# Kernel tuning notes

Hardware: AMD Instinct MI355X
Metric: run time of the kernel (lower is better)

Reference implementation:

```python
import jax, jax.numpy as jnp
import numpy as np

D_MODEL = 2048
D_HID = D_MODEL // 2
NUM_EXPERTS = 16
TOP_K = 2
EPS = 1e-8


def setup_inputs() -> dict:
    key = jax.random.key(0)
    k1, k2, k3, k4, k5 = jax.random.split(key, 5)
    hidden_states = jax.random.normal(k1, (8, 4096, D_MODEL), dtype=jnp.float32)
    # Linear layers: PyTorch stores weight as [out, in]; we keep [in, out] for x @ W.
    s1 = 1.0 / np.sqrt(D_MODEL)
    s2 = 1.0 / np.sqrt(D_HID)
    W1 = jax.random.uniform(k2, (D_MODEL, D_HID), jnp.float32, -s1, s1)
    b1 = jax.random.uniform(k3, (D_HID,), jnp.float32, -s1, s1)
    W2 = jax.random.uniform(k4, (D_HID, NUM_EXPERTS), jnp.float32, -s2, s2)
    b2 = jax.random.uniform(k5, (NUM_EXPERTS,), jnp.float32, -s2, s2)
    return {"hidden_states": hidden_states, "W1": W1, "b1": b1, "W2": W2, "b2": b2}


def reference(hidden_states, W1, b1, W2, b2):
    # 2-layer MLP router (dropout in eval mode -> identity)
    h = jax.nn.relu(jnp.einsum("bsd,dh->bsh", hidden_states, W1) + b1)
    logits = jnp.einsum("bsh,he->bse", h, W2) + b2  # [B, S, E]
    router_probs = jax.nn.softmax(logits, axis=-1)
    top_k_gates, top_k_indices = jax.lax.top_k(router_probs, TOP_K)
    top_k_gates = top_k_gates / (jnp.sum(top_k_gates, axis=-1, keepdims=True) + EPS)
    return top_k_gates, top_k_indices, router_probs
```

## Files before the change

kernel.cpp:

```cpp
#include <hip/hip_runtime.h>
#include <math.h>
#include <stdint.h>

#define TOKENS 32768
#define DM 2048
#define DH 1024
#define NE 16
#define BM 128
#define BN 512
#define NPASS 2
#define BK 32
#define NSTAGE 64
#define RT_TAU 5e-5f
#define FB_TAU 5e-4f
#define XSC 16.0f
#define WSC 64.0f
#define DESC (1.0f/1024.0f)

#define OFF_IDX  (TOKENS * 2)
#define OFF_PROB (TOKENS * 4)

#define WS_LIST 1024
#define WS_WT   132096
#define WIMG_BYTES ((size_t)NSTAGE * NPASS * 65536)
#define WS_NEEDED ((size_t)WS_WT + WIMG_BYTES)
#define RCAP 512

typedef _Float16 f16x8 __attribute__((ext_vector_type(8)));
typedef short    bf16x8 __attribute__((ext_vector_type(8)));
typedef float    f32x16 __attribute__((ext_vector_type(16)));

static __device__ __forceinline__ void gload_lds16(const void* g, void* l) {
    __builtin_amdgcn_global_load_lds(
        (const __attribute__((address_space(1))) void*)g,
        (__attribute__((address_space(3))) void*)l, 16, 0, 0);
}

static __device__ __forceinline__ void cvt_split8(float4 u, float4 v, f16x8& hi, f16x8& lo) {
    float f[8] = {u.x * XSC, u.y * XSC, u.z * XSC, u.w * XSC,
                  v.x * XSC, v.y * XSC, v.z * XSC, v.w * XSC};
    #pragma unroll
    for (int j = 0; j < 8; ++j) {
        _Float16 h = (_Float16)f[j];
        hi[j] = h;
        lo[j] = (_Float16)(f[j] - (float)h);
    }
}

__global__ __launch_bounds__(256)
void prep_w16(const float* __restrict__ W1, char* __restrict__ wimg) {
    const int bid = blockIdx.x;
    const int s = bid >> 1, p = bid & 1;
    char* img = wimg + ((size_t)bid << 16);
    const int tid = threadIdx.x;
    #pragma unroll
    for (int rep = 0; rep < 2; ++rep) {
        const int n = tid + rep * 256;
        #pragma unroll
        for (int q = 0; q < 4; ++q) {
            f16x8 hi, lo;
            #pragma unroll
            for (int j = 0; j < 8; ++j) {
                float ww = W1[(size_t)(s * 32 + q * 8 + j) * DH + p * 512 + n] * WSC;
                _Float16 h = (_Float16)ww;
                hi[j] = h;
                lo[j] = (_Float16)(ww - (float)h);
            }
            *(f16x8*)(img + ((q * 2 + 0) * 512 + n) * 16) = hi;
            *(f16x8*)(img + ((q * 2 + 1) * 512 + n) * 16) = lo;
        }
    }
}

__global__ __launch_bounds__(512, 2)
void router16(const float* __restrict__ x, const char* __restrict__ wimg,
              const float* __restrict__ b1, const float* __restrict__ W2,
              const float* __restrict__ b2, float* __restrict__ out,
              int* __restrict__ cnt, int* __restrict__ list)
{
    __shared__ __align__(16) char smem[163840];
    float* h_lds = (float*)smem;
    float* w2t   = (float*)(smem + 65536);
    float* ls    = (float*)(smem + 73728);
    float* lsred = (float*)smem;

    const int tid  = threadIdx.x;
    const int wid  = tid >> 6;
    const int lane = tid & 63;
    const int l31  = lane & 31;
    const int lh   = lane >> 5;
    const int wm   = wid >> 2;
    const int wn   = wid & 3;
    const int m0   = blockIdx.x * BM;

    const int tq  = tid & 31;
    const int egq = (tid >> 5) & 3;
    const int ns  = tid >> 7;

    const int arow = tid >> 2, kq = tid & 3;

    float lacc[4][4];
    #pragma unroll
    for (int i = 0; i < 4; ++i)
        #pragma unroll
        for (int e = 0; e < 4; ++e) lacc[i][e] = 0.f;

    for (int p = 0; p < NPASS; ++p) {
        f32x16 acc[2][4];
        #pragma unroll
        for (int mf = 0; mf < 2; ++mf)
            #pragma unroll
            for (int nf = 0; nf < 4; ++nf)
                #pragma unroll
                for (int q = 0; q < 16; ++q) acc[mf][nf][q] = 0.f;

        {
            const char* img = wimg + ((size_t)(0 * 2 + p) << 16);
            #pragma unroll
            for (int i = 0; i < 8; ++i) {
                int seg = (wid << 3) + i;
                gload_lds16(img + (seg << 10) + (lane << 4), smem + (seg << 10));
            }
            const float* xp = x + (size_t)(m0 + arow) * DM + kq * 8;
            float4 u = *(const float4*)xp;
            float4 v = *(const float4*)(xp + 4);
            f16x8 hi, lo;
            cvt_split8(u, v, hi, lo);
            char* ab = smem + 131072;
            *(f16x8*)(ab + ((kq * 2 + 0) * 128 + arow) * 16) = hi;
            *(f16x8*)(ab + ((kq * 2 + 1) * 128 + arow) * 16) = lo;
        }
        __syncthreads();

        for (int s = 0; s < NSTAGE; ++s) {
            const int cur = s & 1;
            float4 xu, xv;
            if (s < NSTAGE - 1) {
                const char* img = wimg + ((size_t)((s + 1) * 2 + p) << 16);
                #pragma unroll
                for (int i = 0; i < 8; ++i) {
                    int seg = (wid << 3) + i;
                    gload_lds16(img + (seg << 10) + (lane << 4),
                                smem + ((cur ^ 1) << 16) + (seg << 10));
                }
                const float* xp = x + (size_t)(m0 + arow) * DM + (s + 1) * BK + kq * 8;
                xu = *(const float4*)xp;
                xv = *(const float4*)(xp + 4);
            }
            const char* bb = smem + (cur << 16);
            const char* ab = smem + 131072 + (cur << 14);
            {
                const int q = lh;
                f16x8 ah[2], al[2], bh[4], bl[4];
                #pragma unroll
                for (int mf = 0; mf < 2; ++mf) {
                    int m = wm * 64 + mf * 32 + l31;
                    ah[mf] = *(const f16x8*)(ab + ((q * 2 + 0) * 128 + m) * 16);
                    al[mf] = *(const f16x8*)(ab + ((q * 2 + 1) * 128 + m) * 16);
                }
                #pragma unroll
                for (int nf = 0; nf < 4; ++nf) {
                    int n = wn * 128 + nf * 32 + l31;
                    bh[nf] = *(const f16x8*)(bb + ((q * 2 + 0) * 512 + n) * 16);
                    bl[nf] = *(const f16x8*)(bb + ((q * 2 + 1) * 512 + n) * 16);
                }
                #pragma unroll
                for (int mf = 0; mf < 2; ++mf)
                    #pragma unroll
                    for (int nf = 0; nf < 4; ++nf) {
                        acc[mf][nf] = __builtin_amdgcn_mfma_f32_32x32x16_f16(ah[mf], bh[nf], acc[mf][nf], 0, 0, 0);
                        acc[mf][nf] = __builtin_amdgcn_mfma_f32_32x32x16_f16(ah[mf], bl[nf], acc[mf][nf], 0, 0, 0);
                        acc[mf][nf] = __builtin_amdgcn_mfma_f32_32x32x16_f16(al[mf], bh[nf], acc[mf][nf], 0, 0, 0);
                    }
            }
            if (s < NSTAGE - 1) {
                f16x8 hi, lo;
                cvt_split8(xu, xv, hi, lo);
                char* abn = smem + 131072 + ((cur ^ 1) << 14);
                *(f16x8*)(abn + ((kq * 2 + 0) * 128 + arow) * 16) = hi;
                *(f16x8*)(abn + ((kq * 2 + 1) * 128 + arow) * 16) = lo;
            }
            {
                const int q = 2 + lh;
                f16x8 ah[2], al[2], bh[4], bl[4];
                #pragma unroll
                for (int mf = 0; mf < 2; ++mf) {
                    int m = wm * 64 + mf * 32 + l31;
                    ah[mf] = *(const f16x8*)(ab + ((q * 2 + 0) * 128 + m) * 16);
                    al[mf] = *(const f16x8*)(ab + ((q * 2 + 1) * 128 + m) * 16);
                }
                #pragma unroll
                for (int nf = 0; nf < 4; ++nf) {
                    int n = wn * 128 + nf * 32 + l31;
                    bh[nf] = *(const f16x8*)(bb + ((q * 2 + 0) * 512 + n) * 16);
                    bl[nf] = *(const f16x8*)(bb + ((q * 2 + 1) * 512 + n) * 16);
                }
                #pragma unroll
                for (int mf = 0; mf < 2; ++mf)
                    #pragma unroll
                    for (int nf = 0; nf < 4; ++nf) {
                        acc[mf][nf] = __builtin_amdgcn_mfma_f32_32x32x16_f16(ah[mf], bh[nf], acc[mf][nf], 0, 0, 0);
                        acc[mf][nf] = __builtin_amdgcn_mfma_f32_32x32x16_f16(ah[mf], bl[nf], acc[mf][nf], 0, 0, 0);
                        acc[mf][nf] = __builtin_amdgcn_mfma_f32_32x32x16_f16(al[mf], bh[nf], acc[mf][nf], 0, 0, 0);
                    }
            }
            __syncthreads();
        }
        __syncthreads();

        for (int ch = 0; ch < 4; ++ch) {
            __syncthreads();
            if (wn == ch) {
                #pragma unroll
                for (int nf = 0; nf < 4; ++nf) {
                    int col = nf * 32 + l31;
                    float bb2 = b1[p * BN + ch * 128 + col];
                    #pragma unroll
                    for (int mf = 0; mf < 2; ++mf)
                        #pragma unroll
                        for (int r = 0; r < 16; ++r) {
                            int row = wm * 64 + mf * 32 + (r & 3) + 8 * (r >> 2) + 4 * lh;
                            h_lds[row * 128 + col] = fmaxf(acc[mf][nf][r] * DESC + bb2, 0.f);
                        }
                }
            }
            #pragma unroll
            for (int q = 0; q < 4; ++q) {
                int i = tid * 4 + q;
                int nn = i >> 4, e = i & 15;
                w2t[e * 128 + nn] = W2[(size_t)(p * BN + ch * 128 + nn) * NE + e];
            }
            __syncthreads();
            for (int nn = 0; nn < 32; ++nn) {
                int nL = ns * 32 + ((nn + tq) & 31);
                float hv[4], wv[4];
                #pragma unroll
                for (int i = 0; i < 4; ++i) hv[i] = h_lds[(tq * 4 + i) * 128 + nL];
                #pragma unroll
                for (int e = 0; e < 4; ++e) wv[e] = w2t[(egq * 4 + e) * 128 + nL];
                #pragma unroll
                for (int i = 0; i < 4; ++i)
                    #pragma unroll
                    for (int e = 0; e < 4; ++e)
                        lacc[i][e] = fmaf(hv[i], wv[e], lacc[i][e]);
            }
        }
        __syncthreads();
    }

    #pragma unroll
    for (int i = 0; i < 4; ++i)
        #pragma unroll
        for (int e = 0; e < 4; ++e)
            lsred[((tq * 4 + i) * 16 + egq * 4 + e) * 4 + ns] = lacc[i][e];
    __syncthreads();
    #pragma unroll
    for (int q = 0; q < 4; ++q) {
        int idx = tid * 4 + q;
        int t = idx >> 4, e = idx & 15;
        ls[t * 17 + e] = lsred[idx * 4 + 0] + lsred[idx * 4 + 1] +
                         lsred[idx * 4 + 2] + lsred[idx * 4 + 3] + b2[e];
    }
    __syncthreads();

    if (tid < BM) {
        int t = tid;
        float l[NE]; float mx = -1e30f;
        #pragma unroll
        for (int e = 0; e < NE; ++e) { l[e] = ls[t * 17 + e]; mx = fmaxf(mx, l[e]); }
        float pb[NE]; float ssum = 0.f;
        #pragma unroll
        for (int e = 0; e < NE; ++e) { pb[e] = expf(l[e] - mx); ssum += pb[e]; }
        float inv = 1.f / ssum;
        #pragma unroll
        for (int e = 0; e < NE; ++e) pb[e] *= inv;

        int i1 = 0; float p1 = pb[0];
        #pragma unroll
        for (int e = 1; e < NE; ++e) if (pb[e] > p1) { p1 = pb[e]; i1 = e; }
        int i2 = -1; float p2 = -1.f;
        #pragma unroll
        for (int e = 0; e < NE; ++e) if (e != i1 && pb[e] > p2) { p2 = pb[e]; i2 = e; }
        float p3 = -1.f;
        #pragma unroll
        for (int e = 0; e < NE; ++e) if (e != i1 && e != i2 && pb[e] > p3) p3 = pb[e];

        float denom = p1 + p2 + 1e-8f;
        size_t gt = (size_t)(m0 + t);
        out[gt * 2 + 0] = p1 / denom;
        out[gt * 2 + 1] = p2 / denom;
        out[OFF_IDX + gt * 2 + 0] = (float)i1;
        out[OFF_IDX + gt * 2 + 1] = (float)i2;
        #pragma unroll
        for (int e = 0; e < NE; ++e) out[OFF_PROB + gt * 16 + e] = pb[e];

        if (p1 - p2 < RT_TAU || p2 - p3 < RT_TAU) {
            int k = atomicAdd(cnt, 1);
            list[k] = m0 + t;
        }
    }
}

__global__ __launch_bounds__(256, 4)
void repair_partial(const float* __restrict__ x, const float* __restrict__ W1,
                    const int* __restrict__ cnt, const int* __restrict__ list,
                    float* __restrict__ hpart)
{
    __shared__ float xsl[4][512];
    __shared__ int tokid[4];
    const int tid = threadIdx.x;
    int nrep = cnt[0]; if (nrep > RCAP) nrep = RCAP;
    const int g = blockIdx.x >> 2, ks = blockIdx.x & 3;
    if (g * 4 >= nrep) return;

    if (tid < 4) {
        int j = g * 4 + tid;
        tokid[tid] = list[j < nrep ? j : 0];
    }
    __syncthreads();
    #pragma unroll
    for (int i = 0; i < 2; ++i) {
        int slot = tid + i * 256;
        int t = slot >> 7, c = slot & 127;
        *(float4*)(&xsl[t][c * 4]) =
            *(const float4*)(x + (size_t)tokid[t] * DM + ks * 512 + c * 4);
    }
    __syncthreads();

    float acc[4][4];
    #pragma unroll
    for (int t = 0; t < 4; ++t)
        #pragma unroll
        for (int q = 0; q < 4; ++q) acc[t][q] = 0.f;

    for (int k4 = 0; k4 < 128; ++k4) {
        float4 xv[4];
        #pragma unroll
        for (int t = 0; t < 4; ++t) xv[t] = *(const float4*)(&xsl[t][k4 * 4]);
        #pragma unroll
        for (int kk = 0; kk < 4; ++kk) {
            const float4 w = *(const float4*)(W1 + (size_t)(ks * 512 + k4 * 4 + kk) * DH + tid * 4);
            #pragma unroll
            for (int t = 0; t < 4; ++t) {
                const float a = ((const float*)&xv[t])[kk];
                acc[t][0] = fmaf(a, w.x, acc[t][0]);
                acc[t][1] = fmaf(a, w.y, acc[t][1]);
                acc[t][2] = fmaf(a, w.z, acc[t][2]);
                acc[t][3] = fmaf(a, w.w, acc[t][3]);
            }
        }
    }
    #pragma unroll
    for (int t = 0; t < 4; ++t)
        *(float4*)(hpart + (size_t)(g * 16 + ks * 4 + t) * 1024 + tid * 4) =
            make_float4(acc[t][0], acc[t][1], acc[t][2], acc[t][3]);
}

__global__ __launch_bounds__(256, 2)
void repair_final(const float* __restrict__ hpart, const float* __restrict__ b1,
                  const float* __restrict__ W2, const float* __restrict__ b2,
                  float* __restrict__ out,
                  const int* __restrict__ cnt, const int* __restrict__ list)
{
    __shared__ float hsh[4][DH];
    __shared__ float red[256];
    __shared__ float lg[4][NE];
    __shared__ int tokid[4];
    const int tid = threadIdx.x;
    int nrep = cnt[0]; if (nrep > RCAP) nrep = RCAP;
    const int g = blockIdx.x;
    if (g * 4 >= nrep) return;

    if (tid < 4) {
        int j = g * 4 + tid;
        tokid[tid] = list[j < nrep ? j : 0];
    }
    __syncthreads();
    #pragma unroll
    for (int i = 0; i < 4; ++i) {
        int slot = tid + i * 256;
        int t = slot >> 8, c = slot & 255;
        float4 s0 = *(const float4*)(hpart + (size_t)(g * 16 + 0 * 4 + t) * 1024 + c * 4);
        float4 s1 = *(const float4*)(hpart + (size_t)(g * 16 + 1 * 4 + t) * 1024 + c * 4);
        float4 s2 = *(const float4*)(hpart + (size_t)(g * 16 + 2 * 4 + t) * 1024 + c * 4);
        float4 s3 = *(const float4*)(hpart + (size_t)(g * 16 + 3 * 4 + t) * 1024 + c * 4);
        float4 bv = *(const float4*)(b1 + c * 4);
        float4 h;
        h.x = fmaxf(s0.x + s1.x + s2.x + s3.x + bv.x, 0.f);
        h.y = fmaxf(s0.y + s1.y + s2.y + s3.y + bv.y, 0.f);
        h.z = fmaxf(s0.z + s1.z + s2.z + s3.z + bv.z, 0.f);
        h.w = fmaxf(s0.w + s1.w + s2.w + s3.w + bv.w, 0.f);
        *(float4*)(&hsh[t][c * 4]) = h;
    }
    __syncthreads();
    {
        const int e  = tid & 15;
        const int t  = (tid >> 4) & 3;
        const int sl = tid >> 6;
        float ps = 0.f;
        for (int q = 0; q < 256; ++q) {
            int n = sl * 256 + q;
            ps = fmaf(hsh[t][n], W2[n * NE + e], ps);
        }
        red[tid] = ps;
    }
    __syncthreads();
    if (tid < 64) {
        int t = tid >> 4, e = tid & 15;
        lg[t][e] = b2[e] + red[0 * 64 + t * 16 + e] + red[1 * 64 + t * 16 + e]
                         + red[2 * 64 + t * 16 + e] + red[3 * 64 + t * 16 + e];
    }
    __syncthreads();
    if (tid < 4 && g * 4 + tid < nrep) {
        const int t = tid;
        float l[NE]; float mx = -1e30f;
        #pragma unroll
        for (int e = 0; e < NE; ++e) { l[e] = lg[t][e]; mx = fmaxf(mx, l[e]); }
        float pb[NE]; float ssum = 0.f;
        #pragma unroll
        for (int e = 0; e < NE; ++e) { pb[e] = expf(l[e] - mx); ssum += pb[e]; }
        float inv = 1.f / ssum;
        #pragma unroll
        for (int e = 0; e < NE; ++e) pb[e] *= inv;
        int i1 = 0; float p1 = pb[0];
        #pragma unroll
        for (int e = 1; e < NE; ++e) if (pb[e] > p1) { p1 = pb[e]; i1 = e; }
        int i2 = -1; float p2 = -1.f;
        #pragma unroll
        for (int e = 0; e < NE; ++e) if (e != i1 && pb[e] > p2) { p2 = pb[e]; i2 = e; }
        float denom = p1 + p2 + 1e-8f;
        size_t gt = (size_t)tokid[t];
        out[gt * 2 + 0] = p1 / denom;
        out[gt * 2 + 1] = p2 / denom;
        out[OFF_IDX + gt * 2 + 0] = (float)i1;
        out[OFF_IDX + gt * 2 + 1] = (float)i2;
        #pragma unroll
        for (int e = 0; e < NE; ++e) out[OFF_PROB + gt * 16 + e] = pb[e];
    }
}

__global__ __launch_bounds__(256, 3)
void repair4(const float* __restrict__ x, const float* __restrict__ W1,
             const float* __restrict__ b1, const float* __restrict__ W2,
             const float* __restrict__ b2, float* __restrict__ out,
             const int* __restrict__ cnt, const int* __restrict__ list, int g0)
{
    __shared__ float xsh[4][DM];
    __shared__ float hsh[4][DH];
    __shared__ float red[256];
    __shared__ float lg[4][NE];
    __shared__ int   tokid[4];

    const int tid  = threadIdx.x;
    const int nrep = cnt[0];

    for (int g = g0 + blockIdx.x; g * 4 < nrep; g += gridDim.x) {
        __syncthreads();
        if (tid < 4) {
            int j = g * 4 + tid;
            tokid[tid] = list[j < nrep ? j : 0];
        }
        __syncthreads();
        #pragma unroll
        for (int i = 0; i < 8; ++i) {
            int slot = tid + i * 256;
            int t = slot >> 9, c = slot & 511;
            *(float4*)(&xsh[t][c * 4]) =
                *(const float4*)(x + (size_t)tokid[t] * DM + c * 4);
        }
        __syncthreads();

        float acc[4][4];
        #pragma unroll
        for (int t = 0; t < 4; ++t)
            #pragma unroll
            for (int q = 0; q < 4; ++q) acc[t][q] = 0.f;

        for (int k4 = 0; k4 < DM / 4; ++k4) {
            float4 xv[4];
            #pragma unroll
            for (int t = 0; t < 4; ++t) xv[t] = *(const float4*)(&xsh[t][k4 * 4]);
            #pragma unroll
            for (int kk = 0; kk < 4; ++kk) {
                const float4 w = *(const float4*)(W1 + (size_t)(k4 * 4 + kk) * DH + tid * 4);
                #pragma unroll
                for (int t = 0; t < 4; ++t) {
                    const float a = ((const float*)&xv[t])[kk];
                    acc[t][0] = fmaf(a, w.x, acc[t][0]);
                    acc[t][1] = fmaf(a, w.y, acc[t][1]);
                    acc[t][2] = fmaf(a, w.z, acc[t][2]);
                    acc[t][3] = fmaf(a, w.w, acc[t][3]);
                }
            }
        }
        {
            const float4 bv = *(const float4*)(b1 + tid * 4);
            #pragma unroll
            for (int t = 0; t < 4; ++t) {
                float4 h;
                h.x = fmaxf(acc[t][0] + bv.x, 0.f);
                h.y = fmaxf(acc[t][1] + bv.y, 0.f);
                h.z = fmaxf(acc[t][2] + bv.z, 0.f);
                h.w = fmaxf(acc[t][3] + bv.w, 0.f);
                *(float4*)(&hsh[t][tid * 4]) = h;
            }
        }
        __syncthreads();
        {
            const int e  = tid & 15;
            const int t  = (tid >> 4) & 3;
            const int sl = tid >> 6;
            float ps = 0.f;
            for (int q = 0; q < 256; ++q) {
                int n = sl * 256 + q;
                ps = fmaf(hsh[t][n], W2[n * NE + e], ps);
            }
            red[tid] = ps;
        }
        __syncthreads();
        if (tid < 64) {
            int t = tid >> 4, e = tid & 15;
            lg[t][e] = b2[e] + red[0 * 64 + t * 16 + e] + red[1 * 64 + t * 16 + e]
                             + red[2 * 64 + t * 16 + e] + red[3 * 64 + t * 16 + e];
        }
        __syncthreads();
        if (tid < 4 && g * 4 + tid < nrep) {
            const int t = tid;
            float l[NE]; float mx = -1e30f;
            #pragma unroll
            for (int e = 0; e < NE; ++e) { l[e] = lg[t][e]; mx = fmaxf(mx, l[e]); }
            float pb[NE]; float ssum = 0.f;
            #pragma unroll
            for (int e = 0; e < NE; ++e) { pb[e] = expf(l[e] - mx); ssum += pb[e]; }
            float inv = 1.f / ssum;
            #pragma unroll
            for (int e = 0; e < NE; ++e) pb[e] *= inv;
            int i1 = 0; float p1 = pb[0];
            #pragma unroll
            for (int e = 1; e < NE; ++e) if (pb[e] > p1) { p1 = pb[e]; i1 = e; }
            int i2 = -1; float p2 = -1.f;
            #pragma unroll
            for (int e = 0; e < NE; ++e) if (e != i1 && pb[e] > p2) { p2 = pb[e]; i2 = e; }
            float denom = p1 + p2 + 1e-8f;
            size_t gt = (size_t)tokid[t];
            out[gt * 2 + 0] = p1 / denom;
            out[gt * 2 + 1] = p2 / denom;
            out[OFF_IDX + gt * 2 + 0] = (float)i1;
            out[OFF_IDX + gt * 2 + 1] = (float)i2;
            #pragma unroll
            for (int e = 0; e < NE; ++e) out[OFF_PROB + gt * 16 + e] = pb[e];
        }
    }
}

__global__ __launch_bounds__(512, 2)
void router_fb(const float* __restrict__ x, const float* __restrict__ W1,
               const float* __restrict__ b1, const float* __restrict__ W2,
               const float* __restrict__ b2, float* __restrict__ out,
               int* __restrict__ cnt, int* __restrict__ list)
{
    __shared__ short xs[128 * 64];
    __shared__ short bs[BN * 64];
    __shared__ float w2t[NE * 128];
    __shared__ float ls[128 * 17];

    float* h_lds = (float*)bs;
    float* lsred = (float*)bs;

    const int tid  = threadIdx.x;
    const int wid  = tid >> 6;
    const int lane = tid & 63;
    const int l31  = lane & 31;
    const int lh   = lane >> 5;
    const int sg   = lane & 7;
    const int wm   = wid >> 2;
    const int wn   = wid & 3;
    const int m0   = blockIdx.x * 128;

    const int tq  = tid & 31;
    const int egq = (tid >> 5) & 3;
    const int ns  = tid >> 7;

    float lacc[4][4];
    #pragma unroll
    for (int i = 0; i < 4; ++i)
        #pragma unroll
        for (int e = 0; e < 4; ++e) lacc[i][e] = 0.f;

    const int arow = tid >> 2, kq = tid & 3;
    const int asig = arow & 7;
    const int nloc = (wid << 6) + lane;
    const int sgl  = lane & 7;

    for (int p = 0; p < NPASS; ++p) {
        f32x16 acc[2][4];
        #pragma unroll
        for (int mf = 0; mf < 2; ++mf)
            #pragma unroll
            for (int nf = 0; nf < 4; ++nf)
                #pragma unroll
                for (int q = 0; q < 16; ++q) acc[mf][nf][q] = 0.f;

        for (int s = 0; s < 64; ++s) {
            __syncthreads();
            {
                const float* wp = W1 + (size_t)(s * 32) * DH + p * BN + nloc;
                short* rb = bs + nloc * 64;
                #pragma unroll
                for (int h = 0; h < 2; ++h) {
                    float f[16];
                    #pragma unroll
                    for (int j = 0; j < 16; ++j)
                        f[j] = wp[(size_t)(h * 16 + j) * DH];
                    uint32_t hd[8], ld_[8];
                    #pragma unroll
                    for (int q = 0; q < 8; ++q) {
                        uint32_t u0 = __float_as_uint(f[2 * q]);
                        uint32_t u1 = __float_as_uint(f[2 * q + 1]);
                        hd[q] = (u0 >> 16) | (u1 & 0xFFFF0000u);
                        float r0 = f[2 * q]     - __uint_as_float(u0 & 0xFFFF0000u);
                        float r1 = f[2 * q + 1] - __uint_as_float(u1 & 0xFFFF0000u);
                        ld_[q] = (__float_as_uint(r0) >> 16) | (__float_as_uint(r1) & 0xFFFF0000u);
                    }
                    *(int4*)(rb + (((2 * h + 0) ^ sgl) << 3)) = make_int4(hd[0], hd[1], hd[2], hd[3]);
                    *(int4*)(rb + (((2 * h + 1) ^ sgl) << 3)) = make_int4(hd[4], hd[5], hd[6], hd[7]);
                    *(int4*)(rb + (((4 + 2 * h + 0) ^ sgl) << 3)) = make_int4(ld_[0], ld_[1], ld_[2], ld_[3]);
                    *(int4*)(rb + (((4 + 2 * h + 1) ^ sgl) << 3)) = make_int4(ld_[4], ld_[5], ld_[6], ld_[7]);
                }
            }
            {
                const float* xp = x + (size_t)(m0 + arow) * DM + s * 32 + kq * 8;
                float4 v0 = *(const float4*)xp;
                float4 v1 = *(const float4*)(xp + 4);
                float f[8] = {v0.x, v0.y, v0.z, v0.w, v1.x, v1.y, v1.z, v1.w};
                uint32_t hd[4], ld_[4];
                #pragma unroll
                for (int q = 0; q < 4; ++q) {
                    uint32_t u0 = __float_as_uint(f[2 * q]);
                    uint32_t u1 = __float_as_uint(f[2 * q + 1]);
                    hd[q] = (u0 >> 16) | (u1 & 0xFFFF0000u);
                    float r0 = f[2 * q]     - __uint_as_float(u0 & 0xFFFF0000u);
                    float r1 = f[2 * q + 1] - __uint_as_float(u1 & 0xFFFF0000u);
                    ld_[q] = (__float_as_uint(r0) >> 16) | (__float_as_uint(r1) & 0xFFFF0000u);
                }
                short* ra = xs + arow * 64;
                *(int4*)(ra + ((kq ^ asig) << 3))       = make_int4(hd[0], hd[1], hd[2], hd[3]);
                *(int4*)(ra + (((4 + kq) ^ asig) << 3)) = make_int4(ld_[0], ld_[1], ld_[2], ld_[3]);
            }
            __syncthreads();
            #pragma unroll
            for (int ks = 0; ks < 2; ++ks) {
                bf16x8 a0[2], a1[2], b0[4], b1f[4];
                #pragma unroll
                for (int mf = 0; mf < 2; ++mf) {
                    int base = (wm * 64 + mf * 32 + l31) * 64;
                    a0[mf] = *(const bf16x8*)(xs + base + (((ks * 2 + lh)) ^ sg) * 8);
                    a1[mf] = *(const bf16x8*)(xs + base + (((4 + ks * 2 + lh)) ^ sg) * 8);
                }
                #pragma unroll
                for (int nf = 0; nf < 4; ++nf) {
                    int base = (wn * 128 + nf * 32 + l31) * 64;
                    b0[nf]  = *(const bf16x8*)(bs + base + (((ks * 2 + lh)) ^ sg) * 8);
                    b1f[nf] = *(const bf16x8*)(bs + base + (((4 + ks * 2 + lh)) ^ sg) * 8);
                }
                #pragma unroll
                for (int mf = 0; mf < 2; ++mf)
                    #pragma unroll
                    for (int nf = 0; nf < 4; ++nf) {
                        acc[mf][nf] = __builtin_amdgcn_mfma_f32_32x32x16_bf16(a0[mf], b0[nf],  acc[mf][nf], 0, 0, 0);
                        acc[mf][nf] = __builtin_amdgcn_mfma_f32_32x32x16_bf16(a0[mf], b1f[nf], acc[mf][nf], 0, 0, 0);
                        acc[mf][nf] = __builtin_amdgcn_mfma_f32_32x32x16_bf16(a1[mf], b0[nf],  acc[mf][nf], 0, 0, 0);
                    }
            }
        }

        for (int ch = 0; ch < 4; ++ch) {
            __syncthreads();
            if (wn == ch) {
                #pragma unroll
                for (int nf = 0; nf < 4; ++nf) {
                    int col = nf * 32 + l31;
                    float bb = b1[p * BN + ch * 128 + col];
                    #pragma unroll
                    for (int mf = 0; mf < 2; ++mf)
                        #pragma unroll
                        for (int r = 0; r < 16; ++r) {
                            int row = wm * 64 + mf * 32 + (r & 3) + 8 * (r >> 2) + 4 * lh;
                            h_lds[row * 128 + col] = fmaxf(acc[mf][nf][r] + bb, 0.f);
                        }
                }
            }
            #pragma unroll
            for (int q = 0; q < 4; ++q) {
                int i = tid * 4 + q;
                int nn = i >> 4, e = i & 15;
                w2t[e * 128 + nn] = W2[(size_t)(p * BN + ch * 128 + nn) * NE + e];
            }
            __syncthreads();
            for (int nn = 0; nn < 32; ++nn) {
                int nL = ns * 32 + ((nn + tq) & 31);
                float hv[4], wv[4];
                #pragma unroll
                for (int i = 0; i < 4; ++i) hv[i] = h_lds[(tq * 4 + i) * 128 + nL];
                #pragma unroll
                for (int e = 0; e < 4; ++e) wv[e] = w2t[(egq * 4 + e) * 128 + nL];
                #pragma unroll
                for (int i = 0; i < 4; ++i)
                    #pragma unroll
                    for (int e = 0; e < 4; ++e)
                        lacc[i][e] = fmaf(hv[i], wv[e], lacc[i][e]);
            }
        }
    }

    __syncthreads();
    #pragma unroll
    for (int i = 0; i < 4; ++i)
        #pragma unroll
        for (int e = 0; e < 4; ++e)
            lsred[((tq * 4 + i) * 16 + egq * 4 + e) * 4 + ns] = lacc[i][e];
    __syncthreads();
    #pragma unroll
    for (int q = 0; q < 4; ++q) {
        int idx = tid * 4 + q;
        int t = idx >> 4, e = idx & 15;
        ls[t * 17 + e] = lsred[idx * 4 + 0] + lsred[idx * 4 + 1] +
                         lsred[idx * 4 + 2] + lsred[idx * 4 + 3] + b2[e];
    }
    __syncthreads();

    if (tid < 128) {
        int t = tid;
        float l[NE]; float mx = -1e30f;
        #pragma unroll
        for (int e = 0; e < NE; ++e) { l[e] = ls[t * 17 + e]; mx = fmaxf(mx, l[e]); }
        float pb[NE]; float ssum = 0.f;
        #pragma unroll
        for (int e = 0; e < NE; ++e) { pb[e] = expf(l[e] - mx); ssum += pb[e]; }
        float inv = 1.f / ssum;
        #pragma unroll
        for (int e = 0; e < NE; ++e) pb[e] *= inv;

        int i1 = 0; float p1 = pb[0];
        #pragma unroll
        for (int e = 1; e < NE; ++e) if (pb[e] > p1) { p1 = pb[e]; i1 = e; }
        int i2 = -1; float p2 = -1.f;
        #pragma unroll
        for (int e = 0; e < NE; ++e) if (e != i1 && pb[e] > p2) { p2 = pb[e]; i2 = e; }
        float p3 = -1.f;
        #pragma unroll
        for (int e = 0; e < NE; ++e) if (e != i1 && e != i2 && pb[e] > p3) p3 = pb[e];

        float denom = p1 + p2 + 1e-8f;
        size_t gt = (size_t)(m0 + t);
        out[gt * 2 + 0] = p1 / denom;
        out[gt * 2 + 1] = p2 / denom;
        out[OFF_IDX + gt * 2 + 0] = (float)i1;
        out[OFF_IDX + gt * 2 + 1] = (float)i2;
        #pragma unroll
        for (int e = 0; e < NE; ++e) out[OFF_PROB + gt * 16 + e] = pb[e];

        if (p1 - p2 < FB_TAU || p2 - p3 < FB_TAU) {
            int k = atomicAdd(cnt, 1);
            list[k] = m0 + t;
        }
    }
}

extern "C" void kernel_launch(void* const* d_in, const int* in_sizes, int n_in,
                              void* d_out, int out_size, void* d_ws, size_t ws_size,
                              hipStream_t stream) {
    const float* x  = (const float*)d_in[0];
    const float* W1 = (const float*)d_in[1];
    const float* b1 = (const float*)d_in[2];
    const float* W2 = (const float*)d_in[3];
    const float* b2 = (const float*)d_in[4];
    float* out = (float*)d_out;

    int*   cnt   = (int*)d_ws;
    int*   list  = (int*)((char*)d_ws + WS_LIST);
    char*  wimg  = (char*)d_ws + WS_WT;
    float* hpart = (float*)wimg;

    hipMemsetAsync(cnt, 0, sizeof(int), stream);
    if (ws_size >= WS_NEEDED) {
        hipLaunchKernelGGL(prep_w16, dim3(NSTAGE * NPASS), dim3(256), 0, stream, W1, wimg);
        hipLaunchKernelGGL(router16, dim3(TOKENS / BM), dim3(512), 0, stream,
                           x, wimg, b1, W2, b2, out, cnt, list);
        hipLaunchKernelGGL(repair_partial, dim3(512), dim3(256), 0, stream,
                           x, W1, cnt, list, hpart);
        hipLaunchKernelGGL(repair_final, dim3(128), dim3(256), 0, stream,
                           hpart, b1, W2, b2, out, cnt, list);
        hipLaunchKernelGGL(repair4, dim3(128), dim3(256), 0, stream,
                           x, W1, b1, W2, b2, out, cnt, list, RCAP / 4);
    } else {
        hipLaunchKernelGGL(router_fb, dim3(TOKENS / 128), dim3(512), 0, stream,
                           x, W1, b1, W2, b2, out, cnt, list);
        hipLaunchKernelGGL(repair4, dim3(512), dim3(256), 0, stream,
                           x, W1, b1, W2, b2, out, cnt, list, 0);
    }
}
```

Baseline: 480.9 us.

## Swizzle A-tile LDS layout, stagger k-subslice order across waves, raise MFMA priority

The A tile in LDS is re-laid out row-major with an XOR swizzle on the 16-byte k-segment, to cut LDS bank conflicts on the A-fragment reads and the converted-x writes. Even and odd waves now process the two k-subslices in opposite order, so their LDS traffic and MFMA bursts are staggered. s_setprio(1) wraps the MFMA block so math-issuing waves are favoured by the scheduler. The k-loop body is folded into lambdas, which keeps the code compact but relies on the compiler to inline and unroll them well.

```diff
diff --git a/kernel.cpp b/kernel.cpp
--- a/kernel.cpp
+++ b/kernel.cpp
@@ -92,12 +92,14 @@
     const int wm   = wid >> 2;
     const int wn   = wid & 3;
     const int m0   = blockIdx.x * BM;
+    const int sgm  = l31 & 7;
 
     const int tq  = tid & 31;
     const int egq = (tid >> 5) & 3;
     const int ns  = tid >> 7;
 
     const int arow = tid >> 2, kq = tid & 3;
+    const int asg  = arow & 7;
 
     float lacc[4][4];
     #pragma unroll
@@ -127,8 +129,8 @@
             f16x8 hi, lo;
             cvt_split8(u, v, hi, lo);
             char* ab = smem + 131072;
-            *(f16x8*)(ab + ((kq * 2 + 0) * 128 + arow) * 16) = hi;
-            *(f16x8*)(ab + ((kq * 2 + 1) * 128 + arow) * 16) = lo;
+            *(f16x8*)(ab + (arow * 8 + ((kq * 2 + 0) ^ asg)) * 16) = hi;
+            *(f16x8*)(ab + (arow * 8 + ((kq * 2 + 1) ^ asg)) * 16) = lo;
         }
         __syncthreads();
 
@@ -149,14 +151,15 @@
             }
             const char* bb = smem + (cur << 16);
             const char* ab = smem + 131072 + (cur << 14);
-            {
-                const int q = lh;
+
+            auto do_ks = [&](int qbase) {
+                const int q = qbase + lh;
                 f16x8 ah[2], al[2], bh[4], bl[4];
                 #pragma unroll
                 for (int mf = 0; mf < 2; ++mf) {
                     int m = wm * 64 + mf * 32 + l31;
-                    ah[mf] = *(const f16x8*)(ab + ((q * 2 + 0) * 128 + m) * 16);
-                    al[mf] = *(const f16x8*)(ab + ((q * 2 + 1) * 128 + m) * 16);
+                    ah[mf] = *(const f16x8*)(ab + (m * 8 + ((q * 2 + 0) ^ sgm)) * 16);
+                    al[mf] = *(const f16x8*)(ab + (m * 8 + ((q * 2 + 1) ^ sgm)) * 16);
                 }
                 #pragma unroll
                 for (int nf = 0; nf < 4; ++nf) {
@@ -164,6 +167,7 @@
                     bh[nf] = *(const f16x8*)(bb + ((q * 2 + 0) * 512 + n) * 16);
                     bl[nf] = *(const f16x8*)(bb + ((q * 2 + 1) * 512 + n) * 16);
                 }
+                __builtin_amdgcn_s_setprio(1);
                 #pragma unroll
                 for (int mf = 0; mf < 2; ++mf)
                     #pragma unroll
@@ -172,37 +176,22 @@
                         acc[mf][nf] = __builtin_amdgcn_mfma_f32_32x32x16_f16(ah[mf], bl[nf], acc[mf][nf], 0, 0, 0);
                         acc[mf][nf] = __builtin_amdgcn_mfma_f32_32x32x16_f16(al[mf], bh[nf], acc[mf][nf], 0, 0, 0);
                     }
-            }
-            if (s < NSTAGE - 1) {
-                f16x8 hi, lo;
-                cvt_split8(xu, xv, hi, lo);
-                char* abn = smem + 131072 + ((cur ^ 1) << 14);
-                *(f16x8*)(abn + ((kq * 2 + 0) * 128 + arow) * 16) = hi;
-                *(f16x8*)(abn + ((kq * 2 + 1) * 128 + arow) * 16) = lo;
-            }
-            {
-                const int q = 2 + lh;
-                f16x8 ah[2], al[2], bh[4], bl[4];
-                #pragma unroll
-                for (int mf = 0; mf < 2; ++mf) {
-                    int m = wm * 64 + mf * 32 + l31;
-                    ah[mf] = *(const f16x8*)(ab + ((q * 2 + 0) * 128 + m) * 16);
-                    al[mf] = *(const f16x8*)(ab + ((q * 2 + 1) * 128 + m) * 16);
-                }
-                #pragma unroll
-                for (int nf = 0; nf < 4; ++nf) {
-                    int n = wn * 128 + nf * 32 + l31;
-                    bh[nf] = *(const f16x8*)(bb + ((q * 2 + 0) * 512 + n) * 16);
-                    bl[nf] = *(const f16x8*)(bb + ((q * 2 + 1) * 512 + n) * 16);
-                }
-                #pragma unroll
-                for (int mf = 0; mf < 2; ++mf)
-                    #pragma unroll
-                    for (int nf = 0; nf < 4; ++nf) {
-                        acc[mf][nf] = __builtin_amdgcn_mfma_f32_32x32x16_f16(ah[mf], bh[nf], acc[mf][nf], 0, 0, 0);
-                        acc[mf][nf] = __builtin_amdgcn_mfma_f32_32x32x16_f16(ah[mf], bl[nf], acc[mf][nf], 0, 0, 0);
-                        acc[mf][nf] = __builtin_amdgcn_mfma_f32_32x32x16_f16(al[mf], bh[nf], acc[mf][nf], 0, 0, 0);
-                    }
+                __builtin_amdgcn_s_setprio(0);
+            };
+            auto a_write = [&]() {
+                if (s < NSTAGE - 1) {
+                    f16x8 hi, lo;
+                    cvt_split8(xu, xv, hi, lo);
+                    char* abn = smem + 131072 + ((cur ^ 1) << 14);
+                    *(f16x8*)(abn + (arow * 8 + ((kq * 2 + 0) ^ asg)) * 16) = hi;
+                    *(f16x8*)(abn + (arow * 8 + ((kq * 2 + 1) ^ asg)) * 16) = lo;
+                }
+            };
+
+            if ((wid & 1) == 0) {
+                do_ks(0); a_write(); do_ks(2);
+            } else {
+                do_ks(2); a_write(); do_ks(0);
             }
             __syncthreads();
         }
```

Measured after the change: 599.5 us. +24.7%, slower.
